# Kernel tuning notes

Hardware: AMD Instinct MI355X
Metric: run time of the kernel (lower is better)

The kernel has to match this reference:

```python
import jax, jax.numpy as jnp
import numpy as np

B, S, D_IN, D_OUT, H = 2, 2048, 1024, 1024, 16
HD = D_OUT // H  # head dim = 64


def setup_inputs() -> dict:
    key = jax.random.key(0)
    ks = jax.random.split(key, 9)
    s_in = 1.0 / np.sqrt(D_IN)
    s_out = 1.0 / np.sqrt(D_OUT)
    return {
        "X": jax.random.normal(ks[0], (B, S, D_IN), dtype=jnp.float32),
        "Wq": jax.random.uniform(ks[1], (D_OUT, D_IN), jnp.float32, -s_in, s_in),
        "bq": jax.random.uniform(ks[2], (D_OUT,), jnp.float32, -s_in, s_in),
        "Wk": jax.random.uniform(ks[3], (D_OUT, D_IN), jnp.float32, -s_in, s_in),
        "bk": jax.random.uniform(ks[4], (D_OUT,), jnp.float32, -s_in, s_in),
        "Wv": jax.random.uniform(ks[5], (D_OUT, D_IN), jnp.float32, -s_in, s_in),
        "bv": jax.random.uniform(ks[6], (D_OUT,), jnp.float32, -s_in, s_in),
        "Wo": jax.random.uniform(ks[7], (D_OUT, D_OUT), jnp.float32, -s_out, s_out),
        "bo": jax.random.uniform(ks[8], (D_OUT,), jnp.float32, -s_out, s_out),
    }


def reference(X, Wq, bq, Wk, bk, Wv, bv, Wo, bo):
    scale = jnp.asarray(HD ** 0.5, X.dtype)  # self.dim = sqrt(head_dim)
    q = X @ Wq.T + bq  # [B,S,D_OUT]
    k = X @ Wk.T + bk
    v = X @ Wv.T + bv
    # split heads: b s (h d) -> b h s d
    q = q.reshape(B, S, H, HD).transpose(0, 2, 1, 3)
    k = k.reshape(B, S, H, HD).transpose(0, 2, 1, 3)
    v = v.reshape(B, S, H, HD).transpose(0, 2, 1, 3)
    scores = jnp.einsum('bhsd,bhtd->bhst', q, k) / scale  # [B,H,S,S]
    causal = jnp.triu(jnp.ones((S, S), dtype=bool), k=1)
    scores = jnp.where(causal, -jnp.inf, scores)
    weights = jax.nn.softmax(scores, axis=-1)
    out = jnp.einsum('bhst,bhtd->bhsd', weights, v)  # [B,H,S,HD]
    out = out.transpose(0, 2, 1, 3).reshape(B, S, D_OUT)  # b h s d -> b s (h d)
    return out @ Wo.T + bo
```

## Files before the change

kernel.cpp:

```cpp
#include <hip/hip_runtime.h>
#include <hip/hip_bf16.h>

typedef __bf16 bf16_t;
typedef __bf16 bf16x8 __attribute__((ext_vector_type(8)));
typedef float  f32x4  __attribute__((ext_vector_type(4)));
typedef unsigned short ushort_t;

#define MFMA16(a, b, c) __builtin_amdgcn_mfma_f32_16x16x32_bf16((a), (b), (c), 0, 0, 0)
#define GLDS16(g, l) __builtin_amdgcn_global_load_lds( \
    (const __attribute__((address_space(1))) unsigned int*)(g), \
    (__attribute__((address_space(3))) unsigned int*)(l), 16, 0, 0)

#define WAITCNT_VM(n)  (0x0F70 | (n))
#define WAITCNT_LGKM0  0xC07F

#define MEMFENCE asm volatile("" ::: "memory")

#define SWZ(r) ((((r) >> 1) ^ ((r) >> 3)) & 3)

#define QSCALE 0.18033688f

__global__ __launch_bounds__(256) void cvt_all(
    const void* __restrict__ X,  const void* __restrict__ W0, const void* __restrict__ W1,
    const void* __restrict__ W2, const void* __restrict__ W3,
    const void* __restrict__ c0, const void* __restrict__ c1,
    const void* __restrict__ c2, const void* __restrict__ c3,
    bf16_t* __restrict__ Xb, bf16_t* __restrict__ Wb, float* __restrict__ biasF,
    int* __restrict__ flag)
{
    const int tid  = threadIdx.x;
    const int lane = tid & 63;
    const ushort_t u = ((const ushort_t*)X)[2 * lane];
    const int e = (u >> 7) & 0xFF;
    const int f = (__ballot(e >= 0xA0) != 0ull) ? 1 : 0;

    const int bid = blockIdx.x;
    if (bid >= 4096) {
        if (bid == 4096 && tid == 0) *flag = f;
        const int idx = ((bid - 4096) * 256 + tid) * 8;
        const int w = idx >> 10, off = idx & 1023;
        const void* src = (w == 0) ? c0 : (w == 1) ? c1 : (w == 2) ? c2 : c3;
        #pragma unroll
        for (int r = 0; r < 8; ++r)
            biasF[idx + r] = f ? ((const float*)src)[off + r]
                               : (float)((const bf16_t*)src)[off + r];
        return;
    }

    const long long i = (long long)bid * 2048 + tid * 8;
    const void* src;
    bf16_t* dst;
    long long off;
    if (i < 4194304) { src = X; dst = Xb; off = i; }
    else {
        const int w = (int)((i - 4194304) >> 20);
        off = (i - 4194304) & 1048575;
        src = (w == 0) ? W0 : (w == 1) ? W1 : (w == 2) ? W2 : W3;
        dst = Wb + (size_t)w * 1048576;
    }
    if (f) {
        const float* s = (const float*)src + off;
        const float4 a = *(const float4*)(s);
        const float4 b = *(const float4*)(s + 4);
        bf16x8 o;
        o[0] = (bf16_t)a.x; o[1] = (bf16_t)a.y; o[2] = (bf16_t)a.z; o[3] = (bf16_t)a.w;
        o[4] = (bf16_t)b.x; o[5] = (bf16_t)b.y; o[6] = (bf16_t)b.z; o[7] = (bf16_t)b.w;
        *(bf16x8*)(dst + off) = o;
    } else {
        *(bf16x8*)(dst + off) = *(const bf16x8*)((const bf16_t*)src + off);
    }
}

__global__ __launch_bounds__(512, 2) void gemm256(
    const bf16_t* __restrict__ A,
    const bf16_t* __restrict__ W0, const bf16_t* __restrict__ W1, const bf16_t* __restrict__ W2,
    const float* __restrict__ b0, const float* __restrict__ b1, const float* __restrict__ b2,
    bf16_t* __restrict__ C, bf16_t* __restrict__ Vt)
{
    __shared__ bf16_t Ash[4][256 * 32];
    __shared__ bf16_t Bsh[4][256 * 32];

    const int tid  = threadIdx.x;
    const int wid  = tid >> 6;
    const int lane = tid & 63;
    const int g    = lane >> 4;
    const int c    = lane & 15;

    const int m0  = blockIdx.x * 256;
    const int n0  = blockIdx.y * 256;
    const int mat = n0 >> 10;
    const bf16_t* W  = (mat == 0) ? W0 : (mat == 1) ? W1 : W2;
    const float*  bs = (mat == 0) ? b0 : (mat == 1) ? b1 : b2;
    const int nw = n0 & 1023;

    const int srow = lane >> 2;
    const int sblk = (lane & 3) ^ ((lane >> 3) & 3);
    const bf16_t* Ag = A + (size_t)(m0 + wid * 32 + srow) * 1024 + sblk * 8;
    const bf16_t* Wg = W + (size_t)(nw + wid * 32 + srow) * 1024 + sblk * 8;

    const int waveM = (wid >> 2) * 128;
    const int waveN = (wid & 3) * 64;
    const int fblk  = (g ^ ((c >> 1) & 3)) * 8;

    f32x4 acc[8][4] = {};

    auto stageA = [&](int H, int q) {
        GLDS16(Ag + (size_t)(q * 16) * 1024 + H * 32, &Ash[H & 3][(wid * 32 + q * 16) * 32]);
    };
    auto stageB = [&](int H, int q) {
        GLDS16(Wg + (size_t)(q * 16) * 1024 + H * 32, &Bsh[H & 3][(wid * 32 + q * 16) * 32]);
    };

    for (int H = 0; H < 3; ++H) {
        stageA(H, 0); stageA(H, 1); stageB(H, 0); stageB(H, 1);
    }
    __builtin_amdgcn_s_waitcnt(WAITCNT_VM(8));
    __builtin_amdgcn_s_barrier();
    MEMFENCE;

    #pragma unroll 4
    for (int H = 0; H < 32; ++H) {
        const int buf = H & 3;
        const bf16_t* As = Ash[buf];
        const bf16_t* Bs = Bsh[buf];

        bf16x8 bfr[4], af[8];
        #pragma unroll
        for (int j = 0; j < 4; ++j)
            bfr[j] = *(const bf16x8*)(&Bs[(waveN + j * 16 + c) * 32 + fblk]);
        #pragma unroll
        for (int i = 0; i < 8; ++i)
            af[i] = *(const bf16x8*)(&As[(waveM + i * 16 + c) * 32 + fblk]);

        if (H < 29) { stageA(H + 3, 0); stageA(H + 3, 1); stageB(H + 3, 0); stageB(H + 3, 1); }

        __builtin_amdgcn_s_setprio(1);
        #pragma unroll
        for (int i = 0; i < 8; ++i)
            #pragma unroll
            for (int j = 0; j < 4; ++j)
                acc[i][j] = MFMA16(af[i], bfr[j], acc[i][j]);
        __builtin_amdgcn_s_setprio(0);

        MEMFENCE;
        __builtin_amdgcn_s_waitcnt(WAITCNT_LGKM0);
        if (H < 29)       __builtin_amdgcn_s_waitcnt(WAITCNT_VM(8));
        else if (H == 29) __builtin_amdgcn_s_waitcnt(WAITCNT_VM(4));
        else if (H == 30) __builtin_amdgcn_s_waitcnt(WAITCNT_VM(0));
        __builtin_amdgcn_s_barrier();
        MEMFENCE;
    }

    if (mat == 2) {
        #pragma unroll
        for (int j = 0; j < 4; ++j) {
            const int col  = n0 + waveN + j * 16 + c;
            const int hcol = col & 1023;
            const float bv = bs[hcol];
            const int h = hcol >> 6, d = hcol & 63;
            #pragma unroll
            for (int i = 0; i < 8; ++i) {
                const int row = m0 + waveM + i * 16 + g * 4;
                const int bb = row >> 11, s = row & 2047;
                bf16_t pk[4];
                #pragma unroll
                for (int r = 0; r < 4; ++r) pk[r] = (bf16_t)(acc[i][j][r] + bv);
                *(uint2*)(&Vt[(((size_t)bb * 16 + h) * 64 + d) * 2048 + s]) = *(uint2*)pk;
            }
        }
        return;
    }

    const float os = (mat == 0) ? QSCALE : 1.0f;
    #pragma unroll
    for (int j = 0; j < 4; ++j) {
        const int col = n0 + waveN + j * 16 + c;
        const float bv = bs[col & 1023];
        #pragma unroll
        for (int i = 0; i < 8; ++i) {
            const int row = m0 + waveM + i * 16 + g * 4;
            #pragma unroll
            for (int r = 0; r < 4; ++r)
                C[(size_t)(row + r) * 3072 + col] = (bf16_t)((acc[i][j][r] + bv) * os);
        }
    }
}

template<int TM>
__global__ __launch_bounds__(256, 3) void gemm_nt(
    const bf16_t* __restrict__ A,
    const bf16_t* __restrict__ W0,
    const float* __restrict__ b0,
    void* __restrict__ C, int ldc,
    const int* __restrict__ flag, int is_out)
{
    constexpr int MI = TM / 32;
    __shared__ bf16_t Ash[2][TM * 32];
    __shared__ bf16_t Bsh[2][128 * 32];

    const int f32out = is_out ? *flag : 0;

    const int tid  = threadIdx.x;
    const int wid  = tid >> 6;
    const int lane = tid & 63;
    const int g    = lane >> 4;
    const int c    = lane & 15;

    const int m0  = blockIdx.x * TM;
    const int n0  = blockIdx.y * 128;
    const bf16_t* W  = W0;
    const float*  bs = b0;
    const int nw = n0 & 1023;

    const int srow = lane >> 2;
    const int sblk = (lane & 3) ^ ((lane >> 3) & 3);
    const bf16_t* Ag = A + (size_t)(m0 + wid * (TM / 4) + srow) * 1024 + sblk * 8;
    const bf16_t* Wg = W + (size_t)(nw + wid * 32 + srow) * 1024 + sblk * 8;

    const int waveM = (wid >> 1) * (TM / 2);
    const int waveN = (wid & 1) * 64;

    f32x4 acc[MI][4] = {};
    const int fblk = (g ^ ((c >> 1) & 3)) * 8;

    auto stage = [&](int t) {
        const int k0 = t * 32;
        const int buf = t & 1;
        bf16_t* As = &Ash[buf][(wid * (TM / 4)) * 32];
        bf16_t* Bs = &Bsh[buf][(wid * 32) * 32];
        GLDS16(Ag + k0, As);
        if (TM == 128) GLDS16(Ag + (size_t)16 * 1024 + k0, As + 16 * 32);
        GLDS16(Wg + k0, Bs);
        GLDS16(Wg + (size_t)16 * 1024 + k0, Bs + 16 * 32);
    };

    stage(0);
    __builtin_amdgcn_s_waitcnt(WAITCNT_VM(0));
    __builtin_amdgcn_s_barrier();
    MEMFENCE;

    #pragma unroll 2
    for (int k = 0; k < 32; ++k) {
        const int cur = k & 1;
        bf16x8 af[MI], bfr[4];
        #pragma unroll
        for (int i = 0; i < MI; ++i)
            af[i] = *(const bf16x8*)(&Ash[cur][(waveM + i * 16 + c) * 32 + fblk]);
        #pragma unroll
        for (int j = 0; j < 4; ++j)
            bfr[j] = *(const bf16x8*)(&Bsh[cur][(waveN + j * 16 + c) * 32 + fblk]);

        if (k < 31) stage(k + 1);

        __builtin_amdgcn_s_setprio(1);
        #pragma unroll
        for (int i = 0; i < MI; ++i)
            #pragma unroll
            for (int j = 0; j < 4; ++j)
                acc[i][j] = MFMA16(af[i], bfr[j], acc[i][j]);
        __builtin_amdgcn_s_setprio(0);

        MEMFENCE;
        __builtin_amdgcn_s_waitcnt(WAITCNT_LGKM0);
        if (k < 31) __builtin_amdgcn_s_waitcnt(WAITCNT_VM(0));
        __builtin_amdgcn_s_barrier();
        MEMFENCE;
    }

    #pragma unroll
    for (int j = 0; j < 4; ++j) {
        const int col = n0 + waveN + j * 16 + c;
        const float bv = bs[col & 1023];
        #pragma unroll
        for (int i = 0; i < MI; ++i) {
            const int row = m0 + waveM + i * 16 + g * 4;
            #pragma unroll
            for (int r = 0; r < 4; ++r) {
                const float val = acc[i][j][r] + bv;
                const size_t idx = (size_t)(row + r) * ldc + col;
                if (f32out) ((float*)C)[idx] = val;
                else        ((bf16_t*)C)[idx] = (bf16_t)val;
            }
        }
    }
}

__global__ __launch_bounds__(256, 4) void attn_kernel(
    const bf16_t* __restrict__ QKV, const bf16_t* __restrict__ Vt,
    bf16_t* __restrict__ O)
{
    __shared__ bf16_t Ksh[2][64][32];
    __shared__ bf16_t Vsh[2][64][32];
    __shared__ bf16_t Psh[4][2][16][32];

    const int tid  = threadIdx.x;
    const int wid  = tid >> 6;
    const int lane = tid & 63;
    const int g    = lane >> 4;
    const int c    = lane & 15;

    const int bh = blockIdx.y;
    const int b  = bh >> 4, h = bh & 15;
    const int qt = (bh < 16) ? blockIdx.x : (31 - blockIdx.x);
    const int q0 = qt * 64;
    const int nt = qt + 1;

    bf16x8 aq[2];
    {
        const bf16_t* qp = QKV + (size_t)(b * 2048 + q0 + wid * 16 + c) * 3072 + h * 64;
        aq[0] = *(const bf16x8*)(qp + g * 8);
        aq[1] = *(const bf16x8*)(qp + 32 + g * 8);
    }

    float li[4] = {};
    f32x4 o[4]  = {};

    const int sr = tid >> 2;
    const int j4 = tid & 3;
    const bf16_t* Kg = QKV + (size_t)(b * 2048 + sr) * 3072 + 1024 + h * 64 + j4 * 16;
    const bf16_t* Vg = Vt + ((size_t)bh * 64 + sr) * 2048 + j4 * 16;

    const int ssr = SWZ(sr);
    const int bb0 = j4 * 2, bb1 = bb0 + 1;
    bf16_t* kd0 = &Ksh[bb0 >> 2][sr][((bb0 & 3) ^ ssr) * 8];
    bf16_t* kd1 = &Ksh[bb1 >> 2][sr][((bb1 & 3) ^ ssr) * 8];
    bf16_t* vd0 = &Vsh[bb0 >> 2][sr][((bb0 & 3) ^ ssr) * 8];
    bf16_t* vd1 = &Vsh[bb1 >> 2][sr][((bb1 & 3) ^ ssr) * 8];

    uint4 kr0 = *(const uint4*)(Kg);
    uint4 kr1 = *(const uint4*)(Kg + 8);
    uint4 vr0 = *(const uint4*)(Vg);
    uint4 vr1 = *(const uint4*)(Vg + 8);

    for (int jt = 0; jt < nt; ++jt) {
        *(uint4*)kd0 = kr0;
        *(uint4*)kd1 = kr1;
        *(uint4*)vd0 = vr0;
        *(uint4*)vd1 = vr1;
        __syncthreads();

        if (jt + 1 < nt) {
            const size_t ko = (size_t)(jt + 1) * 64 * 3072;
            kr0 = *(const uint4*)(Kg + ko);
            kr1 = *(const uint4*)(Kg + ko + 8);
            vr0 = *(const uint4*)(Vg + (jt + 1) * 64);
            vr1 = *(const uint4*)(Vg + (jt + 1) * 64 + 8);
        }

        f32x4 s[4] = {};
        __builtin_amdgcn_s_setprio(1);
        #pragma unroll
        for (int n = 0; n < 4; ++n)
            #pragma unroll
            for (int kb = 0; kb < 2; ++kb) {
                const int row = n * 16 + c;
                const bf16x8 kf = *(const bf16x8*)(&Ksh[kb][row][(g ^ SWZ(row)) * 8]);
                s[n] = MFMA16(aq[kb], kf, s[n]);
            }
        __builtin_amdgcn_s_setprio(0);

        if (jt == nt - 1) {
            const int j0 = jt * 64;
            const int qrow = q0 + wid * 16 + g * 4;
            #pragma unroll
            for (int n = 0; n < 4; ++n)
                #pragma unroll
                for (int r = 0; r < 4; ++r)
                    if (j0 + n * 16 + c > qrow + r) s[n][r] = -1e30f;
        }

        #pragma unroll
        for (int n = 0; n < 4; ++n)
            #pragma unroll
            for (int r = 0; r < 4; ++r) {
                const float p = __builtin_amdgcn_exp2f(s[n][r]);
                li[r] += p;
                const int q  = g * 4 + r;
                const int gg = 2 * n + (c >> 3);
                Psh[wid][gg >> 2][q][((gg & 3) ^ SWZ(q)) * 8 + (c & 7)] = (bf16_t)p;
            }
        __builtin_amdgcn_wave_barrier();

        __builtin_amdgcn_s_setprio(1);
        #pragma unroll
        for (int kb = 0; kb < 2; ++kb) {
            const bf16x8 ap = *(const bf16x8*)(&Psh[wid][kb][c][(g ^ SWZ(c)) * 8]);
            #pragma unroll
            for (int d = 0; d < 4; ++d) {
                const int row = d * 16 + c;
                const bf16x8 vf = *(const bf16x8*)(&Vsh[kb][row][(g ^ SWZ(row)) * 8]);
                o[d] = MFMA16(ap, vf, o[d]);
            }
        }
        __builtin_amdgcn_s_setprio(0);
        __syncthreads();
    }

    #pragma unroll
    for (int off = 1; off < 16; off <<= 1)
        #pragma unroll
        for (int r = 0; r < 4; ++r)
            li[r] += __shfl_xor(li[r], off, 64);

    const int orow = b * 2048 + q0 + wid * 16 + g * 4;
    #pragma unroll
    for (int r = 0; r < 4; ++r) {
        const float inv = 1.0f / li[r];
        #pragma unroll
        for (int d = 0; d < 4; ++d)
            O[(size_t)(orow + r) * 1024 + h * 64 + d * 16 + c] = (bf16_t)(o[d][r] * inv);
    }
}

extern "C" void kernel_launch(void* const* d_in, const int* in_sizes, int n_in,
                              void* d_out, int out_size, void* d_ws, size_t ws_size,
                              hipStream_t stream)
{
    const void* X  = d_in[0];
    const void* Wq = d_in[1];  const void* bq = d_in[2];
    const void* Wk = d_in[3];  const void* bk = d_in[4];
    const void* Wv = d_in[5];  const void* bv = d_in[6];
    const void* Wo = d_in[7];  const void* bo = d_in[8];

    int*    flag  = (int*)d_ws;
    float*  biasF = (float*)((char*)d_ws + 16);
    bf16_t* Xb    = (bf16_t*)((char*)d_ws + 16 + 16384);
    bf16_t* Wb    = Xb  + (size_t)4096 * 1024;
    bf16_t* QKV   = Wb  + (size_t)4 * 1024 * 1024;
    bf16_t* Vt    = QKV + (size_t)4096 * 3072;
    bf16_t* Ao    = Vt  + (size_t)4096 * 1024;

    const size_t MW = (size_t)1024 * 1024;

    cvt_all<<<4098, 256, 0, stream>>>(X, Wq, Wk, Wv, Wo, bq, bk, bv, bo,
                                      Xb, Wb, biasF, flag);

    gemm256<<<dim3(16, 12), 512, 0, stream>>>(
        Xb, Wb, Wb + MW, Wb + 2 * MW,
        biasF, biasF + 1024, biasF + 2048, QKV, Vt);
    attn_kernel<<<dim3(32, 32), 256, 0, stream>>>(QKV, Vt, Ao);
    gemm_nt<64><<<dim3(64, 8), 256, 0, stream>>>(
        Ao, Wb + 3 * MW, biasF + 3072, d_out, 1024, flag, 1);
}
```

Measured before the change: 202.1 us.

## Retile QKV GEMM to 256x192 tiles over stacked weights and reorder attention staging

The fused QKV projection GEMM now uses 256x192 output tiles over the contiguous stacked Wq/Wk/Wv buffer, giving a 16x16 grid of 256 blocks instead of 192. This spreads the work more evenly across the CUs. Because 192 rows no longer map to one weight matrix, the epilogue picks the Q scale or the V-transpose path per 16-column group. Four waves issue an extra load, so the wait counts now differ per wave. The attention kernel's K/V staging also changes so each thread loads two 16-byte chunks 32 elements apart, which changes the global access pattern and the LDS swizzle placement.

```diff
diff --git a/kernel.cpp b/kernel.cpp
--- a/kernel.cpp
+++ b/kernel.cpp
@@ -71,14 +71,14 @@
     }
 }
 
-__global__ __launch_bounds__(512, 2) void gemm256(
+__global__ __launch_bounds__(512, 2) void gemm_qkv(
     const bf16_t* __restrict__ A,
-    const bf16_t* __restrict__ W0, const bf16_t* __restrict__ W1, const bf16_t* __restrict__ W2,
-    const float* __restrict__ b0, const float* __restrict__ b1, const float* __restrict__ b2,
+    const bf16_t* __restrict__ Wst,
+    const float* __restrict__ biasAll,
     bf16_t* __restrict__ C, bf16_t* __restrict__ Vt)
 {
     __shared__ bf16_t Ash[4][256 * 32];
-    __shared__ bf16_t Bsh[4][256 * 32];
+    __shared__ bf16_t Bsh[4][192 * 32];
 
     const int tid  = threadIdx.x;
     const int wid  = tid >> 6;
@@ -86,35 +86,33 @@
     const int g    = lane >> 4;
     const int c    = lane & 15;
 
-    const int m0  = blockIdx.x * 256;
-    const int n0  = blockIdx.y * 256;
-    const int mat = n0 >> 10;
-    const bf16_t* W  = (mat == 0) ? W0 : (mat == 1) ? W1 : W2;
-    const float*  bs = (mat == 0) ? b0 : (mat == 1) ? b1 : b2;
-    const int nw = n0 & 1023;
+    const int m0 = blockIdx.x * 256;
+    const int n0 = blockIdx.y * 192;
 
     const int srow = lane >> 2;
     const int sblk = (lane & 3) ^ ((lane >> 3) & 3);
-    const bf16_t* Ag = A + (size_t)(m0 + wid * 32 + srow) * 1024 + sblk * 8;
-    const bf16_t* Wg = W + (size_t)(nw + wid * 32 + srow) * 1024 + sblk * 8;
+    const bf16_t* Ag  = A   + (size_t)(m0 + wid * 32 + srow) * 1024 + sblk * 8;
+    const bf16_t* Wg0 = Wst + (size_t)(n0 + wid * 16 + srow) * 1024 + sblk * 8;
+    const bf16_t* Wg1 = Wst + (size_t)(n0 + 128 + wid * 16 + srow) * 1024 + sblk * 8;
 
     const int waveM = (wid >> 2) * 128;
-    const int waveN = (wid & 3) * 64;
+    const int waveN = (wid & 3) * 48;
     const int fblk  = (g ^ ((c >> 1) & 3)) * 8;
 
-    f32x4 acc[8][4] = {};
-
-    auto stageA = [&](int H, int q) {
-        GLDS16(Ag + (size_t)(q * 16) * 1024 + H * 32, &Ash[H & 3][(wid * 32 + q * 16) * 32]);
+    f32x4 acc[8][3] = {};
+
+    auto stage = [&](int H) {
+        const int buf = H & 3;
+        GLDS16(Ag + H * 32,                      &Ash[buf][(wid * 32) * 32]);
+        GLDS16(Ag + (size_t)16 * 1024 + H * 32,  &Ash[buf][(wid * 32 + 16) * 32]);
+        GLDS16(Wg0 + H * 32,                     &Bsh[buf][(wid * 16) * 32]);
+        if (wid < 4)
+            GLDS16(Wg1 + H * 32,                 &Bsh[buf][(128 + wid * 16) * 32]);
     };
-    auto stageB = [&](int H, int q) {
-        GLDS16(Wg + (size_t)(q * 16) * 1024 + H * 32, &Bsh[H & 3][(wid * 32 + q * 16) * 32]);
-    };
-
-    for (int H = 0; H < 3; ++H) {
-        stageA(H, 0); stageA(H, 1); stageB(H, 0); stageB(H, 1);
-    }
-    __builtin_amdgcn_s_waitcnt(WAITCNT_VM(8));
+
+    stage(0); stage(1); stage(2);
+    if (wid < 4) __builtin_amdgcn_s_waitcnt(WAITCNT_VM(8));
+    else         __builtin_amdgcn_s_waitcnt(WAITCNT_VM(6));
     __builtin_amdgcn_s_barrier();
     MEMFENCE;
 
@@ -124,39 +122,46 @@
         const bf16_t* As = Ash[buf];
         const bf16_t* Bs = Bsh[buf];
 
-        bf16x8 bfr[4], af[8];
-        #pragma unroll
-        for (int j = 0; j < 4; ++j)
+        bf16x8 bfr[3], af[8];
+        #pragma unroll
+        for (int j = 0; j < 3; ++j)
             bfr[j] = *(const bf16x8*)(&Bs[(waveN + j * 16 + c) * 32 + fblk]);
         #pragma unroll
         for (int i = 0; i < 8; ++i)
             af[i] = *(const bf16x8*)(&As[(waveM + i * 16 + c) * 32 + fblk]);
 
-        if (H < 29) { stageA(H + 3, 0); stageA(H + 3, 1); stageB(H + 3, 0); stageB(H + 3, 1); }
+        if (H < 29) stage(H + 3);
 
         __builtin_amdgcn_s_setprio(1);
         #pragma unroll
         for (int i = 0; i < 8; ++i)
             #pragma unroll
-            for (int j = 0; j < 4; ++j)
+            for (int j = 0; j < 3; ++j)
                 acc[i][j] = MFMA16(af[i], bfr[j], acc[i][j]);
         __builtin_amdgcn_s_setprio(0);
 
         MEMFENCE;
         __builtin_amdgcn_s_waitcnt(WAITCNT_LGKM0);
-        if (H < 29)       __builtin_amdgcn_s_waitcnt(WAITCNT_VM(8));
-        else if (H == 29) __builtin_amdgcn_s_waitcnt(WAITCNT_VM(4));
-        else if (H == 30) __builtin_amdgcn_s_waitcnt(WAITCNT_VM(0));
+        if (H < 29) {
+            if (wid < 4) __builtin_amdgcn_s_waitcnt(WAITCNT_VM(8));
+            else         __builtin_amdgcn_s_waitcnt(WAITCNT_VM(6));
+        } else if (H == 29) {
+            if (wid < 4) __builtin_amdgcn_s_waitcnt(WAITCNT_VM(4));
+            else         __builtin_amdgcn_s_waitcnt(WAITCNT_VM(3));
+        } else if (H == 30) {
+            __builtin_amdgcn_s_waitcnt(WAITCNT_VM(0));
+        }
         __builtin_amdgcn_s_barrier();
         MEMFENCE;
     }
 
-    if (mat == 2) {
-        #pragma unroll
-        for (int j = 0; j < 4; ++j) {
-            const int col  = n0 + waveN + j * 16 + c;
-            const int hcol = col & 1023;
-            const float bv = bs[hcol];
+    #pragma unroll
+    for (int j = 0; j < 3; ++j) {
+        const int cg0 = n0 + waveN + j * 16;
+        const int col = cg0 + c;
+        const float bv = biasAll[col];
+        if (cg0 >= 2048) {
+            const int hcol = col - 2048;
             const int h = hcol >> 6, d = hcol & 63;
             #pragma unroll
             for (int i = 0; i < 8; ++i) {
@@ -167,21 +172,15 @@
                 for (int r = 0; r < 4; ++r) pk[r] = (bf16_t)(acc[i][j][r] + bv);
                 *(uint2*)(&Vt[(((size_t)bb * 16 + h) * 64 + d) * 2048 + s]) = *(uint2*)pk;
             }
-        }
-        return;
-    }
-
-    const float os = (mat == 0) ? QSCALE : 1.0f;
-    #pragma unroll
-    for (int j = 0; j < 4; ++j) {
-        const int col = n0 + waveN + j * 16 + c;
-        const float bv = bs[col & 1023];
-        #pragma unroll
-        for (int i = 0; i < 8; ++i) {
-            const int row = m0 + waveM + i * 16 + g * 4;
-            #pragma unroll
-            for (int r = 0; r < 4; ++r)
-                C[(size_t)(row + r) * 3072 + col] = (bf16_t)((acc[i][j][r] + bv) * os);
+        } else {
+            const float os = (cg0 < 1024) ? QSCALE : 1.0f;
+            #pragma unroll
+            for (int i = 0; i < 8; ++i) {
+                const int row = m0 + waveM + i * 16 + g * 4;
+                #pragma unroll
+                for (int r = 0; r < 4; ++r)
+                    C[(size_t)(row + r) * 3072 + col] = (bf16_t)((acc[i][j][r] + bv) * os);
+            }
         }
     }
 }
@@ -317,20 +316,19 @@
 
     const int sr = tid >> 2;
     const int j4 = tid & 3;
-    const bf16_t* Kg = QKV + (size_t)(b * 2048 + sr) * 3072 + 1024 + h * 64 + j4 * 16;
-    const bf16_t* Vg = Vt + ((size_t)bh * 64 + sr) * 2048 + j4 * 16;
-
-    const int ssr = SWZ(sr);
-    const int bb0 = j4 * 2, bb1 = bb0 + 1;
-    bf16_t* kd0 = &Ksh[bb0 >> 2][sr][((bb0 & 3) ^ ssr) * 8];
-    bf16_t* kd1 = &Ksh[bb1 >> 2][sr][((bb1 & 3) ^ ssr) * 8];
-    bf16_t* vd0 = &Vsh[bb0 >> 2][sr][((bb0 & 3) ^ ssr) * 8];
-    bf16_t* vd1 = &Vsh[bb1 >> 2][sr][((bb1 & 3) ^ ssr) * 8];
+    const bf16_t* Kg = QKV + (size_t)(b * 2048 + sr) * 3072 + 1024 + h * 64 + j4 * 8;
+    const bf16_t* Vg = Vt + ((size_t)bh * 64 + sr) * 2048 + j4 * 8;
+
+    const int sp = (j4 ^ SWZ(sr)) * 8;
+    bf16_t* kd0 = &Ksh[0][sr][sp];
+    bf16_t* kd1 = &Ksh[1][sr][sp];
+    bf16_t* vd0 = &Vsh[0][sr][sp];
+    bf16_t* vd1 = &Vsh[1][sr][sp];
 
     uint4 kr0 = *(const uint4*)(Kg);
-    uint4 kr1 = *(const uint4*)(Kg + 8);
+    uint4 kr1 = *(const uint4*)(Kg + 32);
     uint4 vr0 = *(const uint4*)(Vg);
-    uint4 vr1 = *(const uint4*)(Vg + 8);
+    uint4 vr1 = *(const uint4*)(Vg + 32);
 
     for (int jt = 0; jt < nt; ++jt) {
         *(uint4*)kd0 = kr0;
@@ -342,9 +340,9 @@
         if (jt + 1 < nt) {
             const size_t ko = (size_t)(jt + 1) * 64 * 3072;
             kr0 = *(const uint4*)(Kg + ko);
-            kr1 = *(const uint4*)(Kg + ko + 8);
+            kr1 = *(const uint4*)(Kg + ko + 32);
             vr0 = *(const uint4*)(Vg + (jt + 1) * 64);
-            vr1 = *(const uint4*)(Vg + (jt + 1) * 64 + 8);
+            vr1 = *(const uint4*)(Vg + (jt + 1) * 64 + 32);
         }
 
         f32x4 s[4] = {};
@@ -435,9 +433,7 @@
     cvt_all<<<4098, 256, 0, stream>>>(X, Wq, Wk, Wv, Wo, bq, bk, bv, bo,
                                       Xb, Wb, biasF, flag);
 
-    gemm256<<<dim3(16, 12), 512, 0, stream>>>(
-        Xb, Wb, Wb + MW, Wb + 2 * MW,
-        biasF, biasF + 1024, biasF + 2048, QKV, Vt);
+    gemm_qkv<<<dim3(16, 16), 512, 0, stream>>>(Xb, Wb, biasF, QKV, Vt);
     attn_kernel<<<dim3(32, 32), 256, 0, stream>>>(QKV, Vt, Ao);
     gemm_nt<64><<<dim3(64, 8), 256, 0, stream>>>(
         Ao, Wb + 3 * MW, biasF + 3072, d_out, 1024, flag, 1);
```

Result: faster. 194.3 us (-3.9%).
